# Performance work log

Measured on AMD Instinct MI355X. Metric: run time of the kernel, lower is better.

## Reference

```python
import jax, jax.numpy as jnp
import numpy as np

HOP = 512
FAC = 4
FRAME_LEN = FAC * HOP  # 2048
ALPHA = 0.65
BETA = 0.06


def _inverse_stft_window():
    # torch.hann_window (periodic): w[n] = 0.5*(1 - cos(2*pi*n/N))
    n = np.arange(FRAME_LEN)
    w = 0.5 * (1.0 - np.cos(2.0 * np.pi * n / FRAME_LEN))
    denom = w ** 2
    # overlaps = ceil(frame_length / hop) == FAC (frame_length = FAC*HOP exactly)
    denom = denom.reshape(FAC, HOP).sum(axis=0)          # [HOP]
    denom = np.tile(denom, FAC)                          # [FRAME_LEN]
    return (w / denom).astype(np.float32)


def setup_inputs() -> dict:
    key = jax.random.key(0)
    B, F, T = 8, 1024, 2048
    stft_frames = jax.random.normal(key, (B, 2, F, T), dtype=jnp.float32)
    inv_window = jnp.asarray(_inverse_stft_window())
    return {"stft_frames": stft_frames, "inv_window": inv_window}


def reference(stft_frames, inv_window):
    # stft_frames: [B, 2, F, T] (real/imag stacked on dim 1)
    x = jnp.pad(stft_frames, ((0, 0), (0, 0), (0, 1), (0, 0)))  # F -> F+1 (Nyquist bin)
    real = x[:, 0] / BETA   # [B, F+1, T]
    imag = x[:, 1] / BETA
    # denormalize_complex: |x|^(1/alpha) * exp(i * atan2(im, re))
    mag = (real * real + imag * imag) ** (0.5 / ALPHA)
    theta = jnp.arctan2(imag, real)
    spec = jax.lax.complex(mag * jnp.cos(theta), mag * jnp.sin(theta))  # [B, F+1, T]
    frames = jnp.fft.irfft(spec, axis=-2)                 # [B, 2F, T], 2F == FRAME_LEN
    frames = jnp.transpose(frames, (0, 2, 1))             # [B, T, L]
    frames = frames * inv_window[None, None, :]
    B, T, L = frames.shape
    total = (T - 1) * HOP + L
    # vectorized overlap-add (scatter-add replacing the per-frame python loop)
    idx = (jnp.arange(T)[:, None] * HOP + jnp.arange(L)[None, :]).reshape(-1)  # [T*L]
    full = jnp.zeros((B, total), frames.dtype).at[:, idx].add(frames.reshape(B, -1))
    # output_buffer is empty on the first call; chunk = first hop*T samples
    return full[:, : HOP * T]
```

## Files before the change

kernel.cpp:

```cpp
#include <hip/hip_runtime.h>
#include <cstddef>


#define TDIM 2048
#define FDIM 1024
#define TT 8
#define NTOT (512 * 2048)

static constexpr int kBREV[32] = {0,16,8,24,4,20,12,28,2,18,10,26,6,22,14,30,
                                  1,17,9,25,5,21,13,29,3,19,11,27,7,23,15,31};
static constexpr float kTR[16] = {
  1.0f, 0.98078528040323044f, 0.92387953251128674f, 0.83146961230254524f,
  0.70710678118654757f, 0.55557023301960218f, 0.38268343236508978f, 0.19509032201612825f,
  0.0f, -0.19509032201612825f, -0.38268343236508978f, -0.55557023301960218f,
  -0.70710678118654757f, -0.83146961230254524f, -0.92387953251128674f, -0.98078528040323044f};
static constexpr float kTI[16] = {
  0.0f, 0.19509032201612825f, 0.38268343236508978f, 0.55557023301960218f,
  0.70710678118654757f, 0.83146961230254524f, 0.92387953251128674f, 0.98078528040323044f,
  1.0f, 0.98078528040323044f, 0.92387953251128674f, 0.83146961230254524f,
  0.70710678118654757f, 0.55557023301960218f, 0.38268343236508978f, 0.19509032201612825f};
static constexpr float kCC[32] = {
  1.0f, 0.99518472667219693f, 0.98078528040323044f, 0.95694033573220882f,
  0.92387953251128674f, 0.88192126434835505f, 0.83146961230254524f, 0.77301045336273699f,
  0.70710678118654757f, 0.63439328416364549f, 0.55557023301960218f, 0.47139673682599764f,
  0.38268343236508978f, 0.29028467725446233f, 0.19509032201612825f, 0.098017140329560604f,
  0.0f, -0.098017140329560604f, -0.19509032201612825f, -0.29028467725446233f,
  -0.38268343236508978f, -0.47139673682599764f, -0.55557023301960218f, -0.63439328416364549f,
  -0.70710678118654757f, -0.77301045336273699f, -0.83146961230254524f, -0.88192126434835505f,
  -0.92387953251128674f, -0.95694033573220882f, -0.98078528040323044f, -0.99518472667219693f};
static constexpr float kSS[32] = {
  0.0f, 0.098017140329560604f, 0.19509032201612825f, 0.29028467725446233f,
  0.38268343236508978f, 0.47139673682599764f, 0.55557023301960218f, 0.63439328416364549f,
  0.70710678118654757f, 0.77301045336273699f, 0.83146961230254524f, 0.88192126434835505f,
  0.92387953251128674f, 0.95694033573220882f, 0.98078528040323044f, 0.99518472667219693f,
  1.0f, 0.99518472667219693f, 0.98078528040323044f, 0.95694033573220882f,
  0.92387953251128674f, 0.88192126434835505f, 0.83146961230254524f, 0.77301045336273699f,
  0.70710678118654757f, 0.63439328416364549f, 0.55557023301960218f, 0.47139673682599764f,
  0.38268343236508978f, 0.29028467725446233f, 0.19509032201612825f, 0.098017140329560604f};

template <int H>
__device__ __forceinline__ void fft32_stage(float ar[32], float ai[32]) {
  constexpr int TSTEP = 16 / H;
  #pragma unroll
  for (int g = 0; g < 32; g += 2 * H) {
    #pragma unroll
    for (int j = 0; j < H; ++j) {
      const float twr = kTR[j * TSTEP];
      const float twi = kTI[j * TSTEP];
      const int i0 = g + j, i1 = i0 + H;
      const float tr = twr * ar[i1] - twi * ai[i1];
      const float ti = twr * ai[i1] + twi * ar[i1];
      ar[i1] = ar[i0] - tr; ai[i1] = ai[i0] - ti;
      ar[i0] += tr;         ai[i0] += ti;
    }
  }
}

__device__ __forceinline__ void ifft32_core(float ar[32], float ai[32]) {
  fft32_stage<1>(ar, ai);
  fft32_stage<2>(ar, ai);
  fft32_stage<4>(ar, ai);
  fft32_stage<8>(ar, ai);
  fft32_stage<16>(ar, ai);
}

__device__ __forceinline__ float pow_gain(float v, float PE, float KS) {
  return KS * __builtin_amdgcn_exp2f(PE * __builtin_amdgcn_logf(v));
}

__device__ __forceinline__ void denorm4(float4& r, float4& i, float PE, float KS) {
  float g;
  g = pow_gain(r.x * r.x + i.x * i.x, PE, KS); r.x *= g; i.x *= g;
  g = pow_gain(r.y * r.y + i.y * i.y, PE, KS); r.y *= g; i.y *= g;
  g = pow_gain(r.z * r.z + i.z * i.z, PE, KS); r.z *= g; i.z *= g;
  g = pow_gain(r.w * r.w + i.w * i.w, PE, KS); r.w *= g; i.w *= g;
}

template <int SC>
__device__ __forceinline__ int slot_row(int s) {
  return (SC == 0) ? (s < 256 ? s : s + 512) : (s + 256);
}

template <int SC>
__device__ __forceinline__ void stage1_compute(const float* __restrict__ Sri,
                                               int q, int tl, float wc, float ws,
                                               float ar[32], float ai[32]) {
  #pragma unroll
  for (int u = 0; u < 16; ++u) {
    const int k2 = (SC == 0) ? (u < 8 ? u : u + 16) : (u + 8);
    const int slot = q + 32 * u;
    int slotm_zero = 32 * (16 - u);
    if (SC == 0 && u == 0) slotm_zero = 0;
    if (SC == 0 && u == 8) slotm_zero = 512;
    const int slotm_pos = (32 - q) + 32 * (15 - u);
    const int slotm = (q == 0) ? slotm_zero : slotm_pos;

    const float2 s1 = *(const float2*)(Sri + slot * 16 + 2 * tl);
    const float2 s2 = *(const float2*)(Sri + slotm * 16 + 2 * tl);
    const float cs = wc * kCC[k2] - ws * kSS[k2];
    const float sn = ws * kCC[k2] + wc * kSS[k2];
    const float Pre = s1.x + s2.x, Pim = s1.y - s2.y;
    const float Qre = s1.x - s2.x, Qim = s1.y + s2.y;
    const float uu = cs * Qim + sn * Qre;
    const float vv = cs * Qre - sn * Qim;
    float wr = Pre - uu, wi = Pim + vv;
    if (q == 0 && k2 == 0) { wr = s1.x; wi = s1.x; }
    ar[kBREV[k2]] = wr; ai[kBREV[k2]] = wi;
  }
}

#define XC(t, k1, r) ((k1) * 264 + (r) * 8 + (t))
#define FSTR 2054

__global__ __launch_bounds__(256) void istft_fused(const float* __restrict__ in,
                                                   const float* __restrict__ invw,
                                                   float* __restrict__ out) {
  __shared__ float buf[16896];
  float* Sri = buf;
  float* Xc  = buf;
  float* Fh  = buf;

  const int tid = threadIdx.x;
  const int tl  = tid & 7;
  const int q   = tid >> 3;

  const int id   = blockIdx.x;
  const int xcd  = id & 7;
  const int slot = id >> 3;
  const int b    = slot >> 5;
  const int tile = xcd * 32 + (slot & 31);
  const int t0   = tile * TT;

  const float* re_p = in + ((size_t)b * 2 + 0) * ((size_t)FDIM * TDIM);
  const float* im_p = in + ((size_t)b * 2 + 1) * ((size_t)FDIM * TDIM);

  const float KS = (float)(exp((-1.0 / 0.65) * log(0.06)) / 2048.0);
  const float PE = 7.0f / 26.0f;

  const float aq = 3.0679615757712824e-3f * (float)q;
  const float wc = __cosf(aq), ws = __sinf(aq);

  float ar[32], ai[32];

  {
    float4 reA[4], imA[4];
    #pragma unroll
    for (int j = 0; j < 4; ++j) {
      const int f = tid + 256 * j;
      const int s = f >> 1, cg = f & 1;
      const int row = slot_row<0>(s);
      reA[j] = *(const float4*)(re_p + (size_t)row * TDIM + t0 + 4 * cg);
      imA[j] = *(const float4*)(im_p + (size_t)row * TDIM + t0 + 4 * cg);
    }
    float4 exRe, exIm;
    if (tid < 2) {
      exRe = *(const float4*)(re_p + (size_t)256 * TDIM + t0 + 4 * tid);
      exIm = *(const float4*)(im_p + (size_t)256 * TDIM + t0 + 4 * tid);
    }
    #pragma unroll
    for (int j = 0; j < 4; ++j) {
      const int f = tid + 256 * j;
      const int s = f >> 1, cg = f & 1;
      denorm4(reA[j], imA[j], PE, KS);
      const float4 w0 = {reA[j].x, imA[j].x, reA[j].y, imA[j].y};
      const float4 w1 = {reA[j].z, imA[j].z, reA[j].w, imA[j].w};
      *(float4*)(Sri + s * 16 + 8 * cg)     = w0;
      *(float4*)(Sri + s * 16 + 8 * cg + 4) = w1;
    }
    if (tid < 2) {
      denorm4(exRe, exIm, PE, KS);
      const float4 w0 = {exRe.x, exIm.x, exRe.y, exIm.y};
      const float4 w1 = {exRe.z, exIm.z, exRe.w, exIm.w};
      *(float4*)(Sri + 512 * 16 + 8 * tid)     = w0;
      *(float4*)(Sri + 512 * 16 + 8 * tid + 4) = w1;
    }

    float4 reB[4], imB[4];
    #pragma unroll
    for (int j = 0; j < 4; ++j) {
      const int f = tid + 256 * j;
      const int s = f >> 1, cg = f & 1;
      const int row = slot_row<1>(s);
      reB[j] = *(const float4*)(re_p + (size_t)row * TDIM + t0 + 4 * cg);
      imB[j] = *(const float4*)(im_p + (size_t)row * TDIM + t0 + 4 * cg);
    }
    float4 exReB, exImB;
    if (tid < 2) {
      exReB = *(const float4*)(re_p + (size_t)768 * TDIM + t0 + 4 * tid);
      exImB = *(const float4*)(im_p + (size_t)768 * TDIM + t0 + 4 * tid);
    }
    __syncthreads();

    stage1_compute<0>(Sri, q, tl, wc, ws, ar, ai);
    __syncthreads();

    #pragma unroll
    for (int j = 0; j < 4; ++j) {
      const int f = tid + 256 * j;
      const int s = f >> 1, cg = f & 1;
      denorm4(reB[j], imB[j], PE, KS);
      const float4 w0 = {reB[j].x, imB[j].x, reB[j].y, imB[j].y};
      const float4 w1 = {reB[j].z, imB[j].z, reB[j].w, imB[j].w};
      *(float4*)(Sri + s * 16 + 8 * cg)     = w0;
      *(float4*)(Sri + s * 16 + 8 * cg + 4) = w1;
    }
    if (tid < 2) {
      denorm4(exReB, exImB, PE, KS);
      const float4 w0 = {exReB.x, exImB.x, exReB.y, exImB.y};
      const float4 w1 = {exReB.z, exImB.z, exReB.w, exImB.w};
      *(float4*)(Sri + 512 * 16 + 8 * tid)     = w0;
      *(float4*)(Sri + 512 * 16 + 8 * tid + 4) = w1;
    }
    __syncthreads();
    stage1_compute<1>(Sri, q, tl, wc, ws, ar, ai);
    __syncthreads();
  }

  ifft32_core(ar, ai);

  {
    const float aq2 = 6.1359231515425649e-3f * (float)q;
    const float dc = __cosf(aq2), dsn = __sinf(aq2);
    float cs = 1.0f, sn = 0.0f;
    #pragma unroll
    for (int r = 0; r < 32; ++r) {
      const float2 xv = {cs * ar[r] - sn * ai[r], cs * ai[r] + sn * ar[r]};
      *(float2*)(Xc + 2 * XC(tl, q, r)) = xv;
      const float ncs = cs * dc - sn * dsn;
      sn = cs * dsn + sn * dc;
      cs = ncs;
    }
  }
  __syncthreads();
  float zr[32], zi[32];
  #pragma unroll
  for (int i = 0; i < 32; ++i) {
    const float2 zv = *(const float2*)(Xc + 2 * XC(tl, kBREV[i], q));
    zr[i] = zv.x; zi[i] = zv.y;
  }
  __syncthreads();

  ifft32_core(zr, zi);

  #pragma unroll
  for (int s = 0; s < 32; ++s) {
    const int l0 = 2 * q + 64 * s;
    const float2 w2 = *(const float2*)(invw + l0);
    const float2 fv = {zr[s] * w2.x, zi[s] * w2.y};
    *(float2*)(Fh + tl * FSTR + l0) = fv;
  }
  __syncthreads();

  float* ob = out + (size_t)b * NTOT;
  const int j2 = 2 * tid;
  for (int rel = 0; rel < 11; ++rel) {
    const int tp = t0 + rel;
    if (tp > 2047) break;
    float2 v = {0.0f, 0.0f};
    #pragma unroll
    for (int c = 0; c < 4; ++c) {
      const int tt = rel - c;
      if (tt >= 0 && tt < TT) {
        const float2 f = *(const float2*)(Fh + tt * FSTR + j2 + 512 * c);
        v.x += f.x; v.y += f.y;
      }
    }
    const int n = tp * 512 + j2;
    if (rel >= 3 && rel <= 7) {
      *(float2*)(ob + n) = v;
    } else {
      atomicAdd(&ob[n], v.x);
      atomicAdd(&ob[n + 1], v.y);
    }
  }
}

extern "C" void kernel_launch(void* const* d_in, const int* in_sizes, int n_in,
                              void* d_out, int out_size, void* d_ws, size_t ws_size,
                              hipStream_t stream) {
  (void)in_sizes; (void)n_in; (void)d_ws; (void)ws_size;
  const float* in   = (const float*)d_in[0];
  const float* invw = (const float*)d_in[1];
  float* out = (float*)d_out;
  hipMemsetAsync(out, 0, (size_t)out_size * sizeof(float), stream);
  istft_fused<<<dim3(TDIM / TT * 8), 256, 0, stream>>>(in, invw, out);
}
```

Measured before the change: 229.1 us.

## Double frames per block to 16 with 512 threads and split transpose/OLA phases

Each block now handles 16 time frames with 512 threads instead of 8 frames with 256, reusing the same shared-memory buffer by running the mid-FFT transpose and the overlap-add staging in two halves. Overlap-add boundary contributions between the two halves are carried in registers, so the fraction of output samples written with atomics falls and the block count halves. The price is extra barriers, higher register pressure at 512 threads per block, and fewer blocks to spread across CUs.

```diff
diff --git a/kernel.cpp b/kernel.cpp
--- a/kernel.cpp
+++ b/kernel.cpp
@@ -4,8 +4,11 @@
 
 #define TDIM 2048
 #define FDIM 1024
-#define TT 8
+#define TT 16
+#define NTHR 512
 #define NTOT (512 * 2048)
+#define FSTR 2054
+#define XPAD 264
 
 static constexpr int kBREV[32] = {0,16,8,24,4,20,12,28,2,18,10,26,6,22,14,30,
                                   1,17,9,25,5,21,13,29,3,19,11,27,7,23,15,31};
@@ -95,8 +98,8 @@
     const int slotm_pos = (32 - q) + 32 * (15 - u);
     const int slotm = (q == 0) ? slotm_zero : slotm_pos;
 
-    const float2 s1 = *(const float2*)(Sri + slot * 16 + 2 * tl);
-    const float2 s2 = *(const float2*)(Sri + slotm * 16 + 2 * tl);
+    const float2 s1 = *(const float2*)(Sri + slot * 32 + 2 * tl);
+    const float2 s2 = *(const float2*)(Sri + slotm * 32 + 2 * tl);
     const float cs = wc * kCC[k2] - ws * kSS[k2];
     const float sn = ws * kCC[k2] + wc * kSS[k2];
     const float Pre = s1.x + s2.x, Pim = s1.y - s2.y;
@@ -109,26 +112,25 @@
   }
 }
 
-#define XC(t, k1, r) ((k1) * 264 + (r) * 8 + (t))
-#define FSTR 2054
-
-__global__ __launch_bounds__(256) void istft_fused(const float* __restrict__ in,
-                                                   const float* __restrict__ invw,
-                                                   float* __restrict__ out) {
+#define XH(t, k1, rh) ((k1) * XPAD + (rh) * 16 + (t))
+
+__global__ __launch_bounds__(NTHR) void istft_fused(const float* __restrict__ in,
+                                                    const float* __restrict__ invw,
+                                                    float* __restrict__ out) {
   __shared__ float buf[16896];
   float* Sri = buf;
   float* Xc  = buf;
   float* Fh  = buf;
 
   const int tid = threadIdx.x;
-  const int tl  = tid & 7;
-  const int q   = tid >> 3;
+  const int tl  = tid & 15;
+  const int q   = tid >> 4;
 
   const int id   = blockIdx.x;
   const int xcd  = id & 7;
   const int slot = id >> 3;
-  const int b    = slot >> 5;
-  const int tile = xcd * 32 + (slot & 31);
+  const int b    = slot >> 4;
+  const int tile = xcd * 16 + (slot & 15);
   const int t0   = tile * TT;
 
   const float* re_p = in + ((size_t)b * 2 + 0) * ((size_t)FDIM * TDIM);
@@ -146,46 +148,46 @@
     float4 reA[4], imA[4];
     #pragma unroll
     for (int j = 0; j < 4; ++j) {
-      const int f = tid + 256 * j;
-      const int s = f >> 1, cg = f & 1;
+      const int f = tid + NTHR * j;
+      const int s = f >> 2, cg = f & 3;
       const int row = slot_row<0>(s);
       reA[j] = *(const float4*)(re_p + (size_t)row * TDIM + t0 + 4 * cg);
       imA[j] = *(const float4*)(im_p + (size_t)row * TDIM + t0 + 4 * cg);
     }
     float4 exRe, exIm;
-    if (tid < 2) {
+    if (tid < 4) {
       exRe = *(const float4*)(re_p + (size_t)256 * TDIM + t0 + 4 * tid);
       exIm = *(const float4*)(im_p + (size_t)256 * TDIM + t0 + 4 * tid);
     }
     #pragma unroll
     for (int j = 0; j < 4; ++j) {
-      const int f = tid + 256 * j;
-      const int s = f >> 1, cg = f & 1;
+      const int f = tid + NTHR * j;
+      const int s = f >> 2, cg = f & 3;
       denorm4(reA[j], imA[j], PE, KS);
       const float4 w0 = {reA[j].x, imA[j].x, reA[j].y, imA[j].y};
       const float4 w1 = {reA[j].z, imA[j].z, reA[j].w, imA[j].w};
-      *(float4*)(Sri + s * 16 + 8 * cg)     = w0;
-      *(float4*)(Sri + s * 16 + 8 * cg + 4) = w1;
-    }
-    if (tid < 2) {
+      *(float4*)(Sri + s * 32 + 8 * cg)     = w0;
+      *(float4*)(Sri + s * 32 + 8 * cg + 4) = w1;
+    }
+    if (tid < 4) {
       denorm4(exRe, exIm, PE, KS);
       const float4 w0 = {exRe.x, exIm.x, exRe.y, exIm.y};
       const float4 w1 = {exRe.z, exIm.z, exRe.w, exIm.w};
-      *(float4*)(Sri + 512 * 16 + 8 * tid)     = w0;
-      *(float4*)(Sri + 512 * 16 + 8 * tid + 4) = w1;
+      *(float4*)(Sri + 512 * 32 + 8 * tid)     = w0;
+      *(float4*)(Sri + 512 * 32 + 8 * tid + 4) = w1;
     }
 
     float4 reB[4], imB[4];
     #pragma unroll
     for (int j = 0; j < 4; ++j) {
-      const int f = tid + 256 * j;
-      const int s = f >> 1, cg = f & 1;
+      const int f = tid + NTHR * j;
+      const int s = f >> 2, cg = f & 3;
       const int row = slot_row<1>(s);
       reB[j] = *(const float4*)(re_p + (size_t)row * TDIM + t0 + 4 * cg);
       imB[j] = *(const float4*)(im_p + (size_t)row * TDIM + t0 + 4 * cg);
     }
     float4 exReB, exImB;
-    if (tid < 2) {
+    if (tid < 4) {
       exReB = *(const float4*)(re_p + (size_t)768 * TDIM + t0 + 4 * tid);
       exImB = *(const float4*)(im_p + (size_t)768 * TDIM + t0 + 4 * tid);
     }
@@ -196,20 +198,20 @@
 
     #pragma unroll
     for (int j = 0; j < 4; ++j) {
-      const int f = tid + 256 * j;
-      const int s = f >> 1, cg = f & 1;
+      const int f = tid + NTHR * j;
+      const int s = f >> 2, cg = f & 3;
       denorm4(reB[j], imB[j], PE, KS);
       const float4 w0 = {reB[j].x, imB[j].x, reB[j].y, imB[j].y};
       const float4 w1 = {reB[j].z, imB[j].z, reB[j].w, imB[j].w};
-      *(float4*)(Sri + s * 16 + 8 * cg)     = w0;
-      *(float4*)(Sri + s * 16 + 8 * cg + 4) = w1;
-    }
-    if (tid < 2) {
+      *(float4*)(Sri + s * 32 + 8 * cg)     = w0;
+      *(float4*)(Sri + s * 32 + 8 * cg + 4) = w1;
+    }
+    if (tid < 4) {
       denorm4(exReB, exImB, PE, KS);
       const float4 w0 = {exReB.x, exImB.x, exReB.y, exImB.y};
       const float4 w1 = {exReB.z, exImB.z, exReB.w, exImB.w};
-      *(float4*)(Sri + 512 * 16 + 8 * tid)     = w0;
-      *(float4*)(Sri + 512 * 16 + 8 * tid + 4) = w1;
+      *(float4*)(Sri + 512 * 32 + 8 * tid)     = w0;
+      *(float4*)(Sri + 512 * 32 + 8 * tid + 4) = w1;
     }
     __syncthreads();
     stage1_compute<1>(Sri, q, tl, wc, ws, ar, ai);
@@ -218,60 +220,98 @@
 
   ifft32_core(ar, ai);
 
+  float zr[32], zi[32];
   {
     const float aq2 = 6.1359231515425649e-3f * (float)q;
     const float dc = __cosf(aq2), dsn = __sinf(aq2);
     float cs = 1.0f, sn = 0.0f;
     #pragma unroll
-    for (int r = 0; r < 32; ++r) {
+    for (int r = 0; r < 16; ++r) {
       const float2 xv = {cs * ar[r] - sn * ai[r], cs * ai[r] + sn * ar[r]};
-      *(float2*)(Xc + 2 * XC(tl, q, r)) = xv;
+      *(float2*)(Xc + 2 * XH(tl, q, r)) = xv;
       const float ncs = cs * dc - sn * dsn;
       sn = cs * dsn + sn * dc;
       cs = ncs;
     }
+    __syncthreads();
+    if (q < 16) {
+      #pragma unroll
+      for (int i = 0; i < 32; ++i) {
+        const float2 zv = *(const float2*)(Xc + 2 * XH(tl, kBREV[i], q));
+        zr[i] = zv.x; zi[i] = zv.y;
+      }
+    }
+    __syncthreads();
+    #pragma unroll
+    for (int r = 16; r < 32; ++r) {
+      const float2 xv = {cs * ar[r] - sn * ai[r], cs * ai[r] + sn * ar[r]};
+      *(float2*)(Xc + 2 * XH(tl, q, r - 16)) = xv;
+      const float ncs = cs * dc - sn * dsn;
+      sn = cs * dsn + sn * dc;
+      cs = ncs;
+    }
+    __syncthreads();
+    if (q >= 16) {
+      #pragma unroll
+      for (int i = 0; i < 32; ++i) {
+        const float2 zv = *(const float2*)(Xc + 2 * XH(tl, kBREV[i], q - 16));
+        zr[i] = zv.x; zi[i] = zv.y;
+      }
+    }
+    __syncthreads();
+  }
+
+  ifft32_core(zr, zi);
+
+  float* ob = out + (size_t)b * NTOT;
+  float carry[3];
+
+  if (tl < 8) {
+    #pragma unroll
+    for (int s = 0; s < 32; ++s) {
+      const int l0 = 2 * q + 64 * s;
+      const float2 w2 = *(const float2*)(invw + l0);
+      const float2 fv = {zr[s] * w2.x, zi[s] * w2.y};
+      *(float2*)(Fh + tl * FSTR + l0) = fv;
+    }
   }
   __syncthreads();
-  float zr[32], zi[32];
   #pragma unroll
-  for (int i = 0; i < 32; ++i) {
-    const float2 zv = *(const float2*)(Xc + 2 * XC(tl, kBREV[i], q));
-    zr[i] = zv.x; zi[i] = zv.y;
-  }
-  __syncthreads();
-
-  ifft32_core(zr, zi);
-
-  #pragma unroll
-  for (int s = 0; s < 32; ++s) {
-    const int l0 = 2 * q + 64 * s;
-    const float2 w2 = *(const float2*)(invw + l0);
-    const float2 fv = {zr[s] * w2.x, zi[s] * w2.y};
-    *(float2*)(Fh + tl * FSTR + l0) = fv;
-  }
-  __syncthreads();
-
-  float* ob = out + (size_t)b * NTOT;
-  const int j2 = 2 * tid;
   for (int rel = 0; rel < 11; ++rel) {
-    const int tp = t0 + rel;
-    if (tp > 2047) break;
-    float2 v = {0.0f, 0.0f};
+    float v = 0.0f;
     #pragma unroll
     for (int c = 0; c < 4; ++c) {
       const int tt = rel - c;
-      if (tt >= 0 && tt < TT) {
-        const float2 f = *(const float2*)(Fh + tt * FSTR + j2 + 512 * c);
-        v.x += f.x; v.y += f.y;
-      }
-    }
-    const int n = tp * 512 + j2;
-    if (rel >= 3 && rel <= 7) {
-      *(float2*)(ob + n) = v;
-    } else {
-      atomicAdd(&ob[n], v.x);
-      atomicAdd(&ob[n + 1], v.y);
-    }
+      if (tt >= 0 && tt < 8) v += Fh[tt * FSTR + tid + 512 * c];
+    }
+    if (rel < 3)       atomicAdd(&ob[(t0 + rel) * 512 + tid], v);
+    else if (rel <= 7) ob[(t0 + rel) * 512 + tid] = v;
+    else               carry[rel - 8] = v;
+  }
+  __syncthreads();
+  if (tl >= 8) {
+    #pragma unroll
+    for (int s = 0; s < 32; ++s) {
+      const int l0 = 2 * q + 64 * s;
+      const float2 w2 = *(const float2*)(invw + l0);
+      const float2 fv = {zr[s] * w2.x, zi[s] * w2.y};
+      *(float2*)(Fh + (tl - 8) * FSTR + l0) = fv;
+    }
+  }
+  __syncthreads();
+  #pragma unroll
+  for (int rel = 8; rel < 19; ++rel) {
+    const int tp = t0 + rel;
+    if (tp > 2047) continue;
+    float v = (rel <= 10) ? carry[rel - 8] : 0.0f;
+    #pragma unroll
+    for (int c = 0; c < 4; ++c) {
+      const int tt = rel - c;
+      if (tt >= 8 && tt < 16) v += Fh[(tt - 8) * FSTR + tid + 512 * c];
+    }
+    const int n = tp * 512 + tid;
+    if (rel <= 15) ob[n] = v;
+    else atomicAdd(&ob[n], v);
   }
 }
 
@@ -283,5 +323,5 @@
   const float* invw = (const float*)d_in[1];
   float* out = (float*)d_out;
   hipMemsetAsync(out, 0, (size_t)out_size * sizeof(float), stream);
-  istft_fused<<<dim3(TDIM / TT * 8), 256, 0, stream>>>(in, invw, out);
-}
+  istft_fused<<<dim3(TDIM / TT * 8), NTHR, 0, stream>>>(in, invw, out);
+}
```

Result: slower. 254.3 us (+11.0%).
